# Optimization experiments

Measured on AMD Instinct MI355X. Metric: run time of the kernel, lower is better.

## Reference

```python
import jax, jax.numpy as jnp
import numpy as np

N = 50000      # nodes
DIM = 256      # hidden dim
H = 8          # heads
T = 2          # edge types
E = 800000     # edges per edge type
HD = DIM // H  # head dim


def setup_inputs() -> dict:
    key = jax.random.key(0)
    ks = jax.random.split(key, 7)
    return {
        "x": jax.random.normal(ks[0], (N, DIM), jnp.float32),
        "W_qkv": jax.random.normal(ks[1], (DIM, DIM * T * 3), jnp.float32) * 0.02,
        "b_qkv": jax.random.normal(ks[2], (DIM * T * 3,), jnp.float32) * 0.02,
        "W_out": jax.random.normal(ks[3], (T, DIM, DIM), jnp.float32) * 0.02,
        "b_out": jax.random.normal(ks[4], (T, DIM), jnp.float32) * 0.02,
        "edge_src": jax.random.randint(ks[5], (T, E), 0, N, jnp.int32),
        "edge_dst": jax.random.randint(ks[6], (T, E), 0, N, jnp.int32),
    }


def reference(x, W_qkv, b_qkv, W_out, b_out, edge_src, edge_dst):
    n, dim = x.shape
    scale = 1.0 / jnp.sqrt(jnp.float32(HD))
    # qkv: (N, T*H*3*hd) -> (N, T, H, 3, hd); matches torch reshape(-1, H*T, 3*hd)
    # followed by last-dim split into q,k,v and per-type head split.
    qkv = (x @ W_qkv + b_qkv).reshape(n, T, H, 3, HD)
    q = qkv[..., 0, :]  # (N, T, H, hd)
    k = qkv[..., 1, :]
    v = qkv[..., 2, :]

    outs = [x]  # sep=True prepends residual features
    for t in range(T):
        src = edge_src[t]
        dst = edge_dst[t]
        # u_dot_v: per-edge, per-head dot product of k[src] and q[dst]
        s = jnp.einsum('ehd,ehd->eh', k[:, t][src], q[:, t][dst]) * scale  # (E, H)
        # edge_softmax over incoming edges of each destination node
        m = jax.ops.segment_max(s, dst, num_segments=n)      # (N, H)
        p = jnp.exp(s - m[dst])
        z = jax.ops.segment_sum(p, dst, num_segments=n)      # (N, H)
        prob = p / z[dst]                                    # (E, H)
        # u_mul_e_sum: weighted aggregation of source values
        agg = jax.ops.segment_sum(prob[..., None] * v[:, t][src], dst,
                                  num_segments=n).reshape(n, dim)
        outs.append(agg @ W_out[t] + b_out[t])  # dropout p=0 -> identity
    return jnp.concatenate(outs, axis=-1)  # (N, dim*(T+1))
```

## Files before the change

kernel.cpp:

```cpp
#include <hip/hip_runtime.h>

#define NN 50000
#define DIM 256
#define HH 8
#define TT 2
#define EE 800000
#define HDIM 32

#define NPART 98
#define RNODE 512
#define BCAP 12288
#define K1CH 8192
#define K1BLK 98

typedef __attribute__((ext_vector_type(8))) short short8;
typedef __attribute__((ext_vector_type(8))) unsigned short ushort8v;
typedef __attribute__((ext_vector_type(4))) float f32x4;
typedef __attribute__((ext_vector_type(2))) float f32x2;
typedef __attribute__((ext_vector_type(4))) unsigned int u32x4;

typedef __attribute__((address_space(3))) unsigned int u32_lds;
typedef __attribute__((address_space(1))) const unsigned int u32_glb;

__device__ __forceinline__ float bf2f(ushort u) {
    return __uint_as_float(((unsigned)u) << 16);
}
__device__ __forceinline__ ushort f2bf(float f) {
    unsigned u = __float_as_uint(f);
    unsigned r = u + 0x7fffu + ((u >> 16) & 1u);
    return (ushort)(r >> 16);
}

template <bool HI>
__device__ __forceinline__ f32x2 cvtpk8(unsigned w) {
    return __builtin_amdgcn_cvt_pk_f32_fp8((int)w, HI);
}

__global__ void cvt_x_k(const float* __restrict__ x, ushort* __restrict__ xb, int n4) {
    int i = blockIdx.x * blockDim.x + threadIdx.x;
    if (i < n4) {
        float4 v = ((const float4*)x)[i];
        ushort4 o;
        o.x = f2bf(v.x); o.y = f2bf(v.y); o.z = f2bf(v.z); o.w = f2bf(v.w);
        ((ushort4*)xb)[i] = o;
    }
}

__global__ void cvt_wt_k(const float* __restrict__ W, ushort* __restrict__ Wt, int Ncols) {
    int idx = blockIdx.x * blockDim.x + threadIdx.x;
    int total = 256 * Ncols;
    if (idx < total) {
        int k = idx / Ncols;
        int nn = idx - k * Ncols;
        Wt[nn * 256 + k] = f2bf(W[idx]);
    }
}

template <int EPI>
__global__ __launch_bounds__(256) void gemm3_k(
    const ushort* __restrict__ A, const ushort* __restrict__ Bt,
    const float* __restrict__ bias,
    ushort* __restrict__ qo, unsigned char* __restrict__ kvo,
    float* __restrict__ outf, int M, int col_base)
{
    __shared__ ushort As[128 * 64];
    __shared__ ushort Bs[128 * 64];
    const int tid = threadIdx.x;
    const int lane = tid & 63;
    const int w = tid >> 6;
    const int wr = w >> 1, wc = w & 1;
    const int lr = lane & 15;
    const int lq = lane >> 4;
    const int m0 = blockIdx.x * 128;
    const int n0 = blockIdx.y * 128;

    f32x4 acc[4][4];
#pragma unroll
    for (int mt = 0; mt < 4; ++mt)
#pragma unroll
        for (int nt = 0; nt < 4; ++nt) acc[mt][nt] = (f32x4){0.f, 0.f, 0.f, 0.f};

    for (int ks = 0; ks < 256; ks += 64) {
#pragma unroll
        for (int it = 0; it < 4; ++it) {
            int u = tid + it * 256;
            int r = u >> 3, s = u & 7;
            int ss = (s ^ (r & 7)) << 3;
            const ushort* srcA = A + (size_t)(m0 + r) * 256 + ks + ss;
            __builtin_amdgcn_global_load_lds((u32_glb*)srcA,
                (u32_lds*)((char*)As + (u << 4)), 16, 0, 0);
            const ushort* srcB = Bt + (size_t)(n0 + r) * 256 + ks + ss;
            __builtin_amdgcn_global_load_lds((u32_glb*)srcB,
                (u32_lds*)((char*)Bs + (u << 4)), 16, 0, 0);
        }
        __syncthreads();

#pragma unroll
        for (int ku = 0; ku < 2; ++ku) {
            short8 a[4], b[4];
#pragma unroll
            for (int mt = 0; mt < 4; ++mt) {
                int row = wr * 64 + mt * 16 + lr;
                int s = ku * 4 + lq;
                a[mt] = *(const short8*)((const char*)As + row * 128 + (((s ^ (row & 7)) & 7) << 4));
            }
#pragma unroll
            for (int nt = 0; nt < 4; ++nt) {
                int row = wc * 64 + nt * 16 + lr;
                int s = ku * 4 + lq;
                b[nt] = *(const short8*)((const char*)Bs + row * 128 + (((s ^ (row & 7)) & 7) << 4));
            }
#pragma unroll
            for (int mt = 0; mt < 4; ++mt)
#pragma unroll
                for (int nt = 0; nt < 4; ++nt)
                    acc[mt][nt] = __builtin_amdgcn_mfma_f32_16x16x32_bf16(a[mt], b[nt], acc[mt][nt], 0, 0, 0);
        }
        __syncthreads();
    }

#pragma unroll
    for (int mt = 0; mt < 4; ++mt) {
        int rowb = m0 + wr * 64 + mt * 16 + (lq << 2);
#pragma unroll
        for (int nt = 0; nt < 4; ++nt) {
            int col = n0 + wc * 64 + nt * 16 + lr;
            float bv = bias[col];
#pragma unroll
            for (int r2 = 0; r2 < 4; ++r2) {
                int rr = rowb + r2;
                if (rr < M) {
                    float val = acc[mt][nt][r2] + bv;
                    if (EPI == 0) {
                        int t = col / 768;
                        int rem = col - t * 768;
                        int h = rem / 96;
                        int rem2 = rem - h * 96;
                        int s3 = rem2 >> 5;
                        int hd = rem2 & 31;
                        int d = h * 32 + hd;
                        if (s3 == 0) {
                            qo[((size_t)(t * NN + rr)) * 256 + d] = f2bf(val);
                        } else {
                            unsigned by = ((unsigned)__builtin_amdgcn_cvt_pk_fp8_f32(val, val, 0, false)) & 0xffu;
                            size_t off = ((size_t)(t * NN + rr)) * 512 +
                                         ((size_t)(d >> 3) << 4) + (d & 7) + ((s3 == 2) ? 8 : 0);
                            kvo[off] = (unsigned char)by;
                        }
                    } else {
                        outf[(size_t)rr * 768 + col_base + col] = val;
                    }
                }
            }
        }
    }
}

__global__ __launch_bounds__(256) void edge_bucket_k(
    const int* __restrict__ dst, const int* __restrict__ src,
    int* __restrict__ bcursor, uint2* __restrict__ bpair)
{
    int t = blockIdx.x / K1BLK;
    int cb = blockIdx.x - t * K1BLK;
    int base = cb * K1CH;
    const int* dp = dst + (size_t)t * EE;
    const int* sp = src + (size_t)t * EE;
    __shared__ int bcnt[NPART];
    __shared__ int bbase_l[NPART];
    int tid = threadIdx.x;
    if (tid < NPART) bcnt[tid] = 0;
    __syncthreads();
    int lim = EE - base; if (lim > K1CH) lim = K1CH;
#pragma unroll 4
    for (int it = 0; it < K1CH / 256; ++it) {
        int i = it * 256 + tid;
        if (i < lim) atomicAdd(&bcnt[dp[base + i] >> 9], 1);
    }
    __syncthreads();
    if (tid < NPART)
        bbase_l[tid] = atomicAdd(&bcursor[t * NPART + tid], bcnt[tid]);
    __syncthreads();
    if (tid < NPART) bcnt[tid] = 0;
    __syncthreads();
#pragma unroll 4
    for (int it = 0; it < K1CH / 256; ++it) {
        int i = it * 256 + tid;
        if (i < lim) {
            int d = dp[base + i];
            int s = sp[base + i];
            int p = d >> 9;
            int pos = bbase_l[p] + atomicAdd(&bcnt[p], 1);
            if (pos < BCAP)
                bpair[(size_t)(t * NPART + p) * BCAP + pos] = make_uint2((unsigned)s, (unsigned)d);
        }
    }
}

__global__ __launch_bounds__(128) void bucket_scan_k(
    const int* __restrict__ bcursor, int* __restrict__ bbase)
{
    __shared__ int sh[TT][128];
    int tid = threadIdx.x;
    for (int t = 0; t < TT; ++t)
        sh[t][tid] = (tid < NPART) ? bcursor[t * NPART + tid] : 0;
    __syncthreads();
    for (int off = 1; off < 128; off <<= 1) {
        int v0 = (tid >= off) ? sh[0][tid - off] : 0;
        int v1 = (tid >= off) ? sh[1][tid - off] : 0;
        __syncthreads();
        sh[0][tid] += v0;
        sh[1][tid] += v1;
        __syncthreads();
    }
    for (int t = 0; t < TT; ++t)
        if (tid < NPART) bbase[t * NPART + tid] = (tid == 0) ? 0 : sh[t][tid - 1];
}

__global__ __launch_bounds__(512) void bucket_scatter_k(
    const uint2* __restrict__ bpair, const int* __restrict__ bcursor,
    const int* __restrict__ bbase, int* __restrict__ offs, int* __restrict__ srt)
{
    int b = blockIdx.x;
    int t = b / NPART, p = b - t * NPART;
    int lo = p * RNODE;
    int n = bcursor[b]; if (n > BCAP) n = BCAP;
    int gbase = bbase[b];
    const uint2* ep = bpair + (size_t)b * BCAP;
    __shared__ int hist[RNODE];
    __shared__ int scn[RNODE];
    __shared__ int stage[BCAP];
    int tid = threadIdx.x;
    hist[tid] = 0;
    __syncthreads();
    for (int i = tid; i < n; i += 512)
        atomicAdd(&hist[(int)ep[i].y - lo], 1);
    __syncthreads();
    scn[tid] = hist[tid];
    __syncthreads();
    for (int off = 1; off < RNODE; off <<= 1) {
        int v = (tid >= off) ? scn[tid - off] : 0;
        __syncthreads();
        scn[tid] += v;
        __syncthreads();
    }
    int ex = scn[tid] - hist[tid];
    int node = lo + tid;
    if (node < NN) offs[t * (NN + 1) + node] = gbase + ex;
    if (p == NPART - 1 && tid == 0) offs[t * (NN + 1) + NN] = EE;
    hist[tid] = ex;
    __syncthreads();
    for (int i = tid; i < n; i += 512) {
        uint2 e = ep[i];
        int pos = atomicAdd(&hist[(int)e.y - lo], 1);
        stage[pos] = (int)e.x;
    }
    __syncthreads();
    int* so = srt + (size_t)t * EE + gbase;
    for (int i = tid; i < n; i += 512) so[i] = stage[i];
}

__device__ __forceinline__ float f8dot(u32x4 kv, const float* q)
{
    f32x2 c0 = cvtpk8<false>(kv[0]);
    f32x2 c1 = cvtpk8<true>(kv[0]);
    f32x2 c2 = cvtpk8<false>(kv[1]);
    f32x2 c3 = cvtpk8<true>(kv[1]);
    return q[0] * c0[0] + q[1] * c0[1] + q[2] * c1[0] + q[3] * c1[1] +
           q[4] * c2[0] + q[5] * c2[1] + q[6] * c3[0] + q[7] * c3[1];
}

__device__ __forceinline__ void f8acc(float p, u32x4 kv, float* a)
{
    f32x2 c0 = cvtpk8<false>(kv[2]);
    f32x2 c1 = cvtpk8<true>(kv[2]);
    f32x2 c2 = cvtpk8<false>(kv[3]);
    f32x2 c3 = cvtpk8<true>(kv[3]);
    a[0] += p * c0[0]; a[1] += p * c0[1];
    a[2] += p * c1[0]; a[3] += p * c1[1];
    a[4] += p * c2[0]; a[5] += p * c2[1];
    a[6] += p * c3[0]; a[7] += p * c3[1];
}

__global__ __launch_bounds__(256) void attn_k(
    const ushort* __restrict__ q_ws, const unsigned char* __restrict__ kv_ws,
    const int* __restrict__ offs, const int* __restrict__ srt,
    ushort* __restrict__ agg)
{
    int wid = blockIdx.x * 4 + (threadIdx.x >> 6);
    int lane = threadIdx.x & 63;
    int half = lane >> 5;
    int sub = lane & 31;
    int t = wid / NN;
    int node = wid - t * NN;

    const ushort* qp = q_ws + ((size_t)(t * NN + node)) * 256 + sub * 8;
    ushort8v qu = *(const ushort8v*)qp;
    float q[8];
#pragma unroll
    for (int i = 0; i < 8; ++i) q[i] = bf2f(qu[i]);

    int o0 = offs[t * (NN + 1) + node];
    int o1 = offs[t * (NN + 1) + node + 1];
    const int* sp = srt + (size_t)t * EE;
    const unsigned char* kvb = kv_ws + (size_t)t * NN * 512 + sub * 16;

    const float scale = 0.17677669529663689f;
    float zA = 0.f, zB = 0.f;
    float aA[8] = {0.f, 0.f, 0.f, 0.f, 0.f, 0.f, 0.f, 0.f};
    float aB[8] = {0.f, 0.f, 0.f, 0.f, 0.f, 0.f, 0.f, 0.f};

    int j = o0;
    for (; j + 4 <= o1; j += 4) {
        int s0 = sp[j + half];
        int s1 = sp[j + 2 + half];
        u32x4 kv0 = *(const u32x4*)(kvb + (size_t)s0 * 512);
        u32x4 kv1 = *(const u32x4*)(kvb + (size_t)s1 * 512);
        float d0 = f8dot(kv0, q);
        float d1 = f8dot(kv1, q);
        d0 += __shfl_xor(d0, 1); d1 += __shfl_xor(d1, 1);
        d0 += __shfl_xor(d0, 2); d1 += __shfl_xor(d1, 2);
        float p0 = __expf(d0 * scale);
        float p1 = __expf(d1 * scale);
        zA += p0; zB += p1;
        f8acc(p0, kv0, aA);
        f8acc(p1, kv1, aB);
    }
    for (; j < o1; j += 2) {
        int e = j + half;
        int valid = (e < o1) ? 1 : 0;
        int s0 = sp[valid ? e : j];
        u32x4 kv0 = *(const u32x4*)(kvb + (size_t)s0 * 512);
        float d0 = f8dot(kv0, q);
        d0 += __shfl_xor(d0, 1);
        d0 += __shfl_xor(d0, 2);
        float p0 = valid ? __expf(d0 * scale) : 0.f;
        zA += p0;
        f8acc(p0, kv0, aA);
    }

    float z = zA + zB;
    z += __shfl_xor(z, 32);
    float a[8];
#pragma unroll
    for (int i = 0; i < 8; ++i) {
        a[i] = aA[i] + aB[i];
        a[i] += __shfl_xor(a[i], 32);
    }

    if (half == 0) {
        float inv = (z > 0.f) ? 1.0f / z : 0.f;
        ushort8v r;
#pragma unroll
        for (int i = 0; i < 8; ++i) r[i] = f2bf(a[i] * inv);
        *(ushort8v*)(agg + ((size_t)(t * NN + node)) * 256 + sub * 8) = r;
    }
}

__global__ void xcopy_k(const float* __restrict__ x, float* __restrict__ out) {
    int i = blockIdx.x * blockDim.x + threadIdx.x;
    if (i < NN * 64) {
        int n = i >> 6;
        int c = i & 63;
        float4 v = ((const float4*)x)[i];
        *(float4*)(out + (size_t)n * 768 + c * 4) = v;
    }
}

extern "C" void kernel_launch(void* const* d_in, const int* in_sizes, int n_in,
                              void* d_out, int out_size, void* d_ws, size_t ws_size,
                              hipStream_t stream)
{
    const float* x      = (const float*)d_in[0];
    const float* W_qkv  = (const float*)d_in[1];
    const float* b_qkv  = (const float*)d_in[2];
    const float* W_out  = (const float*)d_in[3];
    const float* b_out  = (const float*)d_in[4];
    const int* edge_src = (const int*)d_in[5];
    const int* edge_dst = (const int*)d_in[6];
    float* out = (float*)d_out;

    char* ws = (char*)d_ws;
    size_t off = 0;
    auto carve = [&](size_t bytes) {
        char* p = ws + off;
        off += (bytes + 255) & ~(size_t)255;
        return p;
    };
    ushort* xb    = (ushort*)carve((size_t)NN * DIM * 2);
    ushort* wqkvt = (ushort*)carve((size_t)1536 * 256 * 2);
    ushort* woutt = (ushort*)carve((size_t)TT * 256 * 256 * 2);
    ushort* q_ws  = (ushort*)carve((size_t)TT * NN * 256 * 2);
    unsigned char* kv_ws = (unsigned char*)carve((size_t)TT * NN * 512);
    ushort* aggb  = (ushort*)carve((size_t)TT * NN * 256 * 2);
    int* offs     = (int*)carve((size_t)TT * (NN + 1) * 4);
    int* srt      = (int*)carve((size_t)TT * EE * 4);
    uint2* bpair  = (uint2*)carve((size_t)TT * NPART * BCAP * 8);
    int* bcursor  = (int*)carve((size_t)TT * NPART * 4);
    int* bbase    = (int*)carve((size_t)TT * NPART * 4);

    (void)hipMemsetAsync(bcursor, 0, (size_t)TT * NPART * 4, stream);

    cvt_x_k<<<(NN * DIM / 4 + 255) / 256, 256, 0, stream>>>(x, xb, NN * DIM / 4);
    cvt_wt_k<<<(256 * 1536 + 255) / 256, 256, 0, stream>>>(W_qkv, wqkvt, 1536);
    for (int t = 0; t < TT; ++t)
        cvt_wt_k<<<(256 * 256 + 255) / 256, 256, 0, stream>>>(W_out + (size_t)t * 65536,
                                                              woutt + (size_t)t * 65536, 256);

    gemm3_k<0><<<dim3(391, 12), 256, 0, stream>>>(xb, wqkvt, b_qkv, q_ws, kv_ws,
                                                  nullptr, NN, 0);

    edge_bucket_k<<<TT * K1BLK, 256, 0, stream>>>(edge_dst, edge_src, bcursor, bpair);
    bucket_scan_k<<<1, 128, 0, stream>>>(bcursor, bbase);
    bucket_scatter_k<<<TT * NPART, 512, 0, stream>>>(bpair, bcursor, bbase, offs, srt);

    attn_k<<<(NN * TT) / 4, 256, 0, stream>>>(q_ws, kv_ws, offs, srt, aggb);

    for (int t = 0; t < TT; ++t)
        gemm3_k<1><<<dim3(391, 2), 256, 0, stream>>>(aggb + (size_t)t * NN * 256,
                                                     woutt + (size_t)t * 65536,
                                                     b_out + (size_t)t * 256,
                                                     nullptr, nullptr,
                                                     out, NN, 256 + t * 256);

    xcopy_k<<<(NN * 64 + 255) / 256, 256, 0, stream>>>(x, out);
}
```

Before: 378.4 us.

## Fuse launches, batch output GEMMs, and vectorize attention edge loop with packed math

```diff
diff --git a/kernel.cpp b/kernel.cpp
--- a/kernel.cpp
+++ b/kernel.cpp
@@ -36,23 +36,36 @@
     return __builtin_amdgcn_cvt_pk_f32_fp8((int)w, HI);
 }
 
-__global__ void cvt_x_k(const float* __restrict__ x, ushort* __restrict__ xb, int n4) {
+__global__ void cvt_xout_k(const float* __restrict__ x, ushort* __restrict__ xb,
+                           float* __restrict__ out) {
     int i = blockIdx.x * blockDim.x + threadIdx.x;
-    if (i < n4) {
+    if (i < NN * 64) {
+        int n = i >> 6;
+        int c = i & 63;
         float4 v = ((const float4*)x)[i];
         ushort4 o;
         o.x = f2bf(v.x); o.y = f2bf(v.y); o.z = f2bf(v.z); o.w = f2bf(v.w);
         ((ushort4*)xb)[i] = o;
-    }
-}
-
-__global__ void cvt_wt_k(const float* __restrict__ W, ushort* __restrict__ Wt, int Ncols) {
+        *(float4*)(out + (size_t)n * 768 + c * 4) = v;
+    }
+}
+
+__global__ void cvt_w_k(const float* __restrict__ Wqkv, const float* __restrict__ Wout,
+                        ushort* __restrict__ wqkvt, ushort* __restrict__ woutt) {
     int idx = blockIdx.x * blockDim.x + threadIdx.x;
-    int total = 256 * Ncols;
-    if (idx < total) {
-        int k = idx / Ncols;
-        int nn = idx - k * Ncols;
-        Wt[nn * 256 + k] = f2bf(W[idx]);
+    if (idx < 256 * 1536) {
+        int k = idx / 1536;
+        int nn = idx - k * 1536;
+        wqkvt[nn * 256 + k] = f2bf(Wqkv[idx]);
+    } else {
+        int j = idx - 256 * 1536;
+        if (j < TT * 65536) {
+            int t = j >> 16;
+            int r = j & 65535;
+            int k = r >> 8;
+            int nn = r & 255;
+            woutt[t * 65536 + nn * 256 + k] = f2bf(Wout[t * 65536 + k * 256 + nn]);
+        }
     }
 }
 
@@ -61,7 +74,7 @@
     const ushort* __restrict__ A, const ushort* __restrict__ Bt,
     const float* __restrict__ bias,
     ushort* __restrict__ qo, unsigned char* __restrict__ kvo,
-    float* __restrict__ outf, int M, int col_base)
+    float* __restrict__ outf, int M)
 {
     __shared__ ushort As[128 * 64];
     __shared__ ushort Bs[128 * 64];
@@ -72,7 +85,18 @@
     const int lr = lane & 15;
     const int lq = lane >> 4;
     const int m0 = blockIdx.x * 128;
-    const int n0 = blockIdx.y * 128;
+
+    int n0, col_base = 0, tsel = 0;
+    if (EPI == 0) {
+        n0 = blockIdx.y * 128;
+    } else {
+        tsel = blockIdx.y >> 1;
+        n0 = (blockIdx.y & 1) * 128;
+        col_base = 256 + tsel * 256;
+    }
+    const ushort* A_  = (EPI == 0) ? A  : A  + (size_t)tsel * NN * 256;
+    const ushort* Bt_ = (EPI == 0) ? Bt : Bt + (size_t)tsel * 65536;
+    const float* bias_ = (EPI == 0) ? bias : bias + tsel * 256;
 
     f32x4 acc[4][4];
 #pragma unroll
@@ -86,10 +110,10 @@
             int u = tid + it * 256;
             int r = u >> 3, s = u & 7;
             int ss = (s ^ (r & 7)) << 3;
-            const ushort* srcA = A + (size_t)(m0 + r) * 256 + ks + ss;
+            const ushort* srcA = A_ + (size_t)(m0 + r) * 256 + ks + ss;
             __builtin_amdgcn_global_load_lds((u32_glb*)srcA,
                 (u32_lds*)((char*)As + (u << 4)), 16, 0, 0);
-            const ushort* srcB = Bt + (size_t)(n0 + r) * 256 + ks + ss;
+            const ushort* srcB = Bt_ + (size_t)(n0 + r) * 256 + ks + ss;
             __builtin_amdgcn_global_load_lds((u32_glb*)srcB,
                 (u32_lds*)((char*)Bs + (u << 4)), 16, 0, 0);
         }
@@ -125,7 +149,7 @@
 #pragma unroll
         for (int nt = 0; nt < 4; ++nt) {
             int col = n0 + wc * 64 + nt * 16 + lr;
-            float bv = bias[col];
+            float bv = bias_[col];
 #pragma unroll
             for (int r2 = 0; r2 < 4; ++r2) {
                 int rr = rowb + r2;
@@ -259,26 +283,22 @@
     for (int i = tid; i < n; i += 512) so[i] = stage[i];
 }
 
-__device__ __forceinline__ float f8dot(u32x4 kv, const float* q)
-{
-    f32x2 c0 = cvtpk8<false>(kv[0]);
-    f32x2 c1 = cvtpk8<true>(kv[0]);
-    f32x2 c2 = cvtpk8<false>(kv[1]);
-    f32x2 c3 = cvtpk8<true>(kv[1]);
-    return q[0] * c0[0] + q[1] * c0[1] + q[2] * c1[0] + q[3] * c1[1] +
-           q[4] * c2[0] + q[5] * c2[1] + q[6] * c3[0] + q[7] * c3[1];
-}
-
-__device__ __forceinline__ void f8acc(float p, u32x4 kv, float* a)
-{
-    f32x2 c0 = cvtpk8<false>(kv[2]);
-    f32x2 c1 = cvtpk8<true>(kv[2]);
-    f32x2 c2 = cvtpk8<false>(kv[3]);
-    f32x2 c3 = cvtpk8<true>(kv[3]);
-    a[0] += p * c0[0]; a[1] += p * c0[1];
-    a[2] += p * c1[0]; a[3] += p * c1[1];
-    a[4] += p * c2[0]; a[5] += p * c2[1];
-    a[6] += p * c3[0]; a[7] += p * c3[1];
+__device__ __forceinline__ float f8dot2(u32x4 kv, const f32x2* q2)
+{
+    f32x2 dd = q2[0] * cvtpk8<false>(kv[0]);
+    dd += q2[1] * cvtpk8<true>(kv[0]);
+    dd += q2[2] * cvtpk8<false>(kv[1]);
+    dd += q2[3] * cvtpk8<true>(kv[1]);
+    return dd[0] + dd[1];
+}
+
+__device__ __forceinline__ void f8acc2(float p, u32x4 kv, f32x2* a2)
+{
+    f32x2 p2 = {p, p};
+    a2[0] += p2 * cvtpk8<false>(kv[2]);
+    a2[1] += p2 * cvtpk8<true>(kv[2]);
+    a2[2] += p2 * cvtpk8<false>(kv[3]);
+    a2[3] += p2 * cvtpk8<true>(kv[3]);
 }
 
 __global__ __launch_bounds__(256) void attn_k(
@@ -295,9 +315,10 @@
 
     const ushort* qp = q_ws + ((size_t)(t * NN + node)) * 256 + sub * 8;
     ushort8v qu = *(const ushort8v*)qp;
-    float q[8];
-#pragma unroll
-    for (int i = 0; i < 8; ++i) q[i] = bf2f(qu[i]);
+    f32x2 q2[4];
+#pragma unroll
+    for (int i = 0; i < 4; ++i)
+        q2[i] = (f32x2){bf2f(qu[2 * i]), bf2f(qu[2 * i + 1])};
 
     int o0 = offs[t * (NN + 1) + node];
     int o1 = offs[t * (NN + 1) + node + 1];
@@ -306,46 +327,76 @@
 
     const float scale = 0.17677669529663689f;
     float zA = 0.f, zB = 0.f;
-    float aA[8] = {0.f, 0.f, 0.f, 0.f, 0.f, 0.f, 0.f, 0.f};
-    float aB[8] = {0.f, 0.f, 0.f, 0.f, 0.f, 0.f, 0.f, 0.f};
+    f32x2 aA[4] = {{0.f,0.f},{0.f,0.f},{0.f,0.f},{0.f,0.f}};
+    f32x2 aB[4] = {{0.f,0.f},{0.f,0.f},{0.f,0.f},{0.f,0.f}};
 
     int j = o0;
+    for (; j + 8 <= o1; j += 8) {
+        int s0 = sp[j + half];
+        int s1 = sp[j + 2 + half];
+        int s2 = sp[j + 4 + half];
+        int s3 = sp[j + 6 + half];
+        u32x4 kv0 = *(const u32x4*)(kvb + (size_t)s0 * 512);
+        u32x4 kv1 = *(const u32x4*)(kvb + (size_t)s1 * 512);
+        u32x4 kv2 = *(const u32x4*)(kvb + (size_t)s2 * 512);
+        u32x4 kv3 = *(const u32x4*)(kvb + (size_t)s3 * 512);
+        float d0 = f8dot2(kv0, q2);
+        float d1 = f8dot2(kv1, q2);
+        float d2 = f8dot2(kv2, q2);
+        float d3 = f8dot2(kv3, q2);
+        d0 += __shfl_xor(d0, 1); d1 += __shfl_xor(d1, 1);
+        d2 += __shfl_xor(d2, 1); d3 += __shfl_xor(d3, 1);
+        d0 += __shfl_xor(d0, 2); d1 += __shfl_xor(d1, 2);
+        d2 += __shfl_xor(d2, 2); d3 += __shfl_xor(d3, 2);
+        float p0 = __expf(d0 * scale);
+        float p1 = __expf(d1 * scale);
+        float p2 = __expf(d2 * scale);
+        float p3 = __expf(d3 * scale);
+        zA += p0 + p2; zB += p1 + p3;
+        f8acc2(p0, kv0, aA);
+        f8acc2(p1, kv1, aB);
+        f8acc2(p2, kv2, aA);
+        f8acc2(p3, kv3, aB);
+    }
     for (; j + 4 <= o1; j += 4) {
         int s0 = sp[j + half];
         int s1 = sp[j + 2 + half];
         u32x4 kv0 = *(const u32x4*)(kvb + (size_t)s0 * 512);
         u32x4 kv1 = *(const u32x4*)(kvb + (size_t)s1 * 512);
-        float d0 = f8dot(kv0, q);
-        float d1 = f8dot(kv1, q);
+        float d0 = f8dot2(kv0, q2);
+        float d1 = f8dot2(kv1, q2);
         d0 += __shfl_xor(d0, 1); d1 += __shfl_xor(d1, 1);
         d0 += __shfl_xor(d0, 2); d1 += __shfl_xor(d1, 2);
         float p0 = __expf(d0 * scale);
         float p1 = __expf(d1 * scale);
         zA += p0; zB += p1;
-        f8acc(p0, kv0, aA);
-        f8acc(p1, kv1, aB);
+        f8acc2(p0, kv0, aA);
+        f8acc2(p1, kv1, aB);
     }
     for (; j < o1; j += 2) {
         int e = j + half;
         int valid = (e < o1) ? 1 : 0;
         int s0 = sp[valid ? e : j];
         u32x4 kv0 = *(const u32x4*)(kvb + (size_t)s0 * 512);
-        float d0 = f8dot(kv0, q);
+        float d0 = f8dot2(kv0, q2);
         d0 += __shfl_xor(d0, 1);
         d0 += __shfl_xor(d0, 2);
         float p0 = valid ? __expf(d0 * scale) : 0.f;
         zA += p0;
-        f8acc(p0, kv0, aA);
+        f8acc2(p0, kv0, aA);
     }
 
     float z = zA + zB;
     z += __shfl_xor(z, 32);
     float a[8];
 #pragma unroll
-    for (int i = 0; i < 8; ++i) {
-        a[i] = aA[i] + aB[i];
-        a[i] += __shfl_xor(a[i], 32);
-    }
+    for (int i = 0; i < 4; ++i) {
+        f32x2 s2 = aA[i] + aB[i];
+        a[2 * i]     = s2[0];
+        a[2 * i + 1] = s2[1];
+    }
+#pragma unroll
+    for (int i = 0; i < 8; ++i) a[i] += __shfl_xor(a[i], 32);
 
     if (half == 0) {
         float inv = (z > 0.f) ? 1.0f / z : 0.f;
@@ -353,16 +404,6 @@
 #pragma unroll
         for (int i = 0; i < 8; ++i) r[i] = f2bf(a[i] * inv);
         *(ushort8v*)(agg + ((size_t)(t * NN + node)) * 256 + sub * 8) = r;
-    }
-}
-
-__global__ void xcopy_k(const float* __restrict__ x, float* __restrict__ out) {
-    int i = blockIdx.x * blockDim.x + threadIdx.x;
-    if (i < NN * 64) {
-        int n = i >> 6;
-        int c = i & 63;
-        float4 v = ((const float4*)x)[i];
-        *(float4*)(out + (size_t)n * 768 + c * 4) = v;
     }
 }
 
@@ -400,14 +441,12 @@
 
     (void)hipMemsetAsync(bcursor, 0, (size_t)TT * NPART * 4, stream);
 
-    cvt_x_k<<<(NN * DIM / 4 + 255) / 256, 256, 0, stream>>>(x, xb, NN * DIM / 4);
-    cvt_wt_k<<<(256 * 1536 + 255) / 256, 256, 0, stream>>>(W_qkv, wqkvt, 1536);
-    for (int t = 0; t < TT; ++t)
-        cvt_wt_k<<<(256 * 256 + 255) / 256, 256, 0, stream>>>(W_out + (size_t)t * 65536,
-                                                              woutt + (size_t)t * 65536, 256);
+    cvt_xout_k<<<(NN * 64 + 255) / 256, 256, 0, stream>>>(x, xb, out);
+    cvt_w_k<<<(256 * 1536 + TT * 65536 + 255) / 256, 256, 0, stream>>>(W_qkv, W_out,
+                                                                       wqkvt, woutt);
 
     gemm3_k<0><<<dim3(391, 12), 256, 0, stream>>>(xb, wqkvt, b_qkv, q_ws, kv_ws,
-                                                  nullptr, NN, 0);
+                                                  nullptr, NN);
 
     edge_bucket_k<<<TT * K1BLK, 256, 0, stream>>>(edge_dst, edge_src, bcursor, bpair);
     bucket_scan_k<<<1, 128, 0, stream>>>(bcursor, bbase);
@@ -415,12 +454,6 @@
 
     attn_k<<<(NN * TT) / 4, 256, 0, stream>>>(q_ws, kv_ws, offs, srt, aggb);
 
-    for (int t = 0; t < TT; ++t)
-        gemm3_k<1><<<dim3(391, 2), 256, 0, stream>>>(aggb + (size_t)t * NN * 256,
-                                                     woutt + (size_t)t * 65536,
-                                                     b_out + (size_t)t * 256,
-                                                     nullptr, nullptr,
-                                                     out, NN, 256 + t * 256);
-
-    xcopy_k<<<(NN * 64 + 255) / 256, 256, 0, stream>>>(x, out);
-}
+    gemm3_k<1><<<dim3(391, 4), 256, 0, stream>>>(aggb, woutt, b_out,
+                                                 nullptr, nullptr, out, NN);
+}
```

Result: faster. 368.3 us (-2.7%).
